# Optimization experiments

Hardware: AMD Instinct MI355X
Metric: run time of the kernel (lower is better)

The kernel has to match this reference:

```python
import jax, jax.numpy as jnp
import numpy as np

ELEM, EMBD, WIN = 128, 128, 128

def setup_inputs() -> dict:
    key = jax.random.key(0)
    ks = jax.random.split(key, 7)
    s = 1.0 / np.sqrt(ELEM)
    return {
        "x": jax.random.normal(ks[0], (8, 16384, ELEM), dtype=jnp.float32),
        "Wq": jax.random.uniform(ks[1], (EMBD, ELEM), jnp.float32, -s, s),
        "bq": jax.random.uniform(ks[2], (EMBD,), jnp.float32, -s, s),
        "Wk": jax.random.uniform(ks[3], (EMBD, ELEM), jnp.float32, -s, s),
        "bk": jax.random.uniform(ks[4], (EMBD,), jnp.float32, -s, s),
        "Wv": jax.random.uniform(ks[5], (EMBD, ELEM), jnp.float32, -s, s),
        "bv": jax.random.uniform(ks[6], (EMBD,), jnp.float32, -s, s),
    }

def reference(x, Wq, bq, Wk, bk, Wv, bv):
    N, S, E = x.shape
    P = S // WIN
    xp = x.reshape(N, P, WIN, E)  # [N,P,W,E]
    q = jnp.einsum('npwe,de->npwd', xp, Wq) + bq
    k = jnp.einsum('npwe,de->npwd', xp, Wk) + bk
    v = jnp.einsum('npwe,de->npwd', xp, Wv) + bv
    # note: original applies NO 1/sqrt(d) scaling
    scores = jnp.einsum('npwd,npud->npwu', q, k)  # [N,P,W,W]
    attn = jax.nn.softmax(scores, axis=-1)
    out = jnp.einsum('npwu,npud->npwd', attn, v)
    return out.reshape(N, S, EMBD)
```

## Files before the change

kernel.cpp:

```cpp
#include <hip/hip_runtime.h>

#define LDSP 136

typedef _Float16 h8 __attribute__((ext_vector_type(8)));
typedef _Float16 h4 __attribute__((ext_vector_type(4)));
typedef float    f4 __attribute__((ext_vector_type(4)));
typedef float    fx16 __attribute__((ext_vector_type(16)));

__global__ void prep(const float* __restrict__ Wq, const float* __restrict__ Wk,
                     const float* __restrict__ bq, _Float16* __restrict__ Mt,
                     float* __restrict__ ck) {
    int idx = blockIdx.x * 256 + threadIdx.x;
    int e = idx & 127, f = idx >> 7;
    float a0 = 0.f, a1 = 0.f, a2 = 0.f, a3 = 0.f;
    for (int d = 0; d < 128; d += 4) {
        a0 += Wk[(d + 0) * 128 + f] * Wq[(d + 0) * 128 + e];
        a1 += Wk[(d + 1) * 128 + f] * Wq[(d + 1) * 128 + e];
        a2 += Wk[(d + 2) * 128 + f] * Wq[(d + 2) * 128 + e];
        a3 += Wk[(d + 3) * 128 + f] * Wq[(d + 3) * 128 + e];
    }
    Mt[idx] = (_Float16)((a0 + a1) + (a2 + a3));

    if (blockIdx.x == 0 && threadIdx.x < 128) {
        int t = threadIdx.x;
        float c0 = 0.f, c1 = 0.f, c2 = 0.f, c3 = 0.f;
        for (int d = 0; d < 128; d += 4) {
            c0 += bq[d + 0] * Wk[(d + 0) * 128 + t];
            c1 += bq[d + 1] * Wk[(d + 1) * 128 + t];
            c2 += bq[d + 2] * Wk[(d + 2) * 128 + t];
            c3 += bq[d + 3] * Wk[(d + 3) * 128 + t];
        }
        ck[t] = (c0 + c1) + (c2 + c3);
    }
}

__global__ __launch_bounds__(512, 2) void attn(
    const float* __restrict__ x, const _Float16* __restrict__ Mt,
    const float* __restrict__ Wv, const float* __restrict__ ck,
    const float* __restrict__ bv, float* __restrict__ out) {
    __shared__ _Float16 Xs[128 * LDSP];
    __shared__ _Float16 Ts[128 * LDSP];
    __shared__ _Float16 Vs[128 * LDSP];
    __shared__ float2   Sm[256];

    const int tid  = threadIdx.x;
    const int wv   = tid >> 6;
    const int lane = tid & 63;
    const int l32  = lane & 31;
    const int hi   = lane >> 5;
    const int hv   = wv & 1;
    const int t4   = wv >> 1;

    h8 mtf[8], wvf[8];
#pragma unroll
    for (int e0 = 0; e0 < 8; ++e0) {
        mtf[e0] = *(const h8*)(Mt + (t4 * 32 + l32) * 128 + e0 * 16 + hi * 8);
        const float* wp = Wv + (t4 * 32 + l32) * 128 + e0 * 16 + hi * 8;
        f4 w0 = *(const f4*)wp;
        f4 w1 = *(const f4*)(wp + 4);
        wvf[e0] = (h8){(_Float16)w0.x, (_Float16)w0.y, (_Float16)w0.z, (_Float16)w0.w,
                       (_Float16)w1.x, (_Float16)w1.y, (_Float16)w1.z, (_Float16)w1.w};
    }
    const float bvv = bv[t4 * 32 + l32];

    const size_t base0 = (size_t)blockIdx.x * 4 * (128 * 128);

    f4 pf[8];
#pragma unroll
    for (int j = 0; j < 8; ++j)
        pf[j] = *(const f4*)(x + base0 + 4 * tid + 2048 * j);

    for (int it = 0; it < 4; ++it) {
#pragma unroll
        for (int j = 0; j < 8; ++j) {
            int idx = 4 * tid + 2048 * j;
            int row = idx >> 7, col = idx & 127;
            f4 f = pf[j];
            h4 h = {(_Float16)f.x, (_Float16)f.y, (_Float16)f.z, (_Float16)f.w};
            *(h4*)(&Xs[row * LDSP + col]) = h;
        }
        __syncthreads();

        h8 xf0[8], xf1[8];
        fx16 accT0, accT1;
        {
            f4 ckv[4];
#pragma unroll
            for (int run = 0; run < 4; ++run)
                ckv[run] = *(const f4*)(ck + t4 * 32 + run * 8 + 4 * hi);
#pragma unroll
            for (int r = 0; r < 16; ++r) accT0[r] = ckv[r >> 2][r & 3];
            accT1 = accT0;
        }
#pragma unroll
        for (int e0 = 0; e0 < 8; ++e0) {
            xf0[e0] = *(const h8*)(&Xs[(hv * 64 + l32) * LDSP + e0 * 16 + hi * 8]);
            xf1[e0] = *(const h8*)(&Xs[(hv * 64 + 32 + l32) * LDSP + e0 * 16 + hi * 8]);
            accT0 = __builtin_amdgcn_mfma_f32_32x32x16_f16(mtf[e0], xf0[e0], accT0, 0, 0, 0);
            accT1 = __builtin_amdgcn_mfma_f32_32x32x16_f16(mtf[e0], xf1[e0], accT1, 0, 0, 0);
        }
#pragma unroll
        for (int run = 0; run < 4; ++run) {
            h4 h0 = {(_Float16)accT0[run * 4 + 0], (_Float16)accT0[run * 4 + 1],
                     (_Float16)accT0[run * 4 + 2], (_Float16)accT0[run * 4 + 3]};
            *(h4*)(&Ts[(hv * 64 + l32) * LDSP + t4 * 32 + run * 8 + 4 * hi]) = h0;
            h4 h1 = {(_Float16)accT1[run * 4 + 0], (_Float16)accT1[run * 4 + 1],
                     (_Float16)accT1[run * 4 + 2], (_Float16)accT1[run * 4 + 3]};
            *(h4*)(&Ts[(hv * 64 + 32 + l32) * LDSP + t4 * 32 + run * 8 + 4 * hi]) = h1;
        }

        fx16 accV0, accV1;
#pragma unroll
        for (int r = 0; r < 16; ++r) accV0[r] = bvv;
        accV1 = accV0;
#pragma unroll
        for (int e0 = 0; e0 < 8; ++e0) {
            accV0 = __builtin_amdgcn_mfma_f32_32x32x16_f16(xf0[e0], wvf[e0], accV0, 0, 0, 0);
            accV1 = __builtin_amdgcn_mfma_f32_32x32x16_f16(xf1[e0], wvf[e0], accV1, 0, 0, 0);
        }
#pragma unroll
        for (int run = 0; run < 4; ++run) {
            h4 g0 = {(_Float16)accV0[run * 4 + 0], (_Float16)accV0[run * 4 + 1],
                     (_Float16)accV0[run * 4 + 2], (_Float16)accV0[run * 4 + 3]};
            *(h4*)(&Vs[(t4 * 32 + l32) * LDSP + hv * 64 + run * 8 + 4 * hi]) = g0;
            h4 g1 = {(_Float16)accV1[run * 4 + 0], (_Float16)accV1[run * 4 + 1],
                     (_Float16)accV1[run * 4 + 2], (_Float16)accV1[run * 4 + 3]};
            *(h4*)(&Vs[(t4 * 32 + l32) * LDSP + hv * 64 + 32 + run * 8 + 4 * hi]) = g1;
        }
        __syncthreads();

        if (it < 3) {
            const float* nx = x + base0 + (size_t)(it + 1) * (128 * 128);
#pragma unroll
            for (int j = 0; j < 8; ++j)
                pf[j] = *(const f4*)(nx + 4 * tid + 2048 * j);
        }

        fx16 s0, s1;
#pragma unroll
        for (int r = 0; r < 16; ++r) s0[r] = 0.f;
        s1 = s0;
#pragma unroll
        for (int f0 = 0; f0 < 8; ++f0) {
            h8 tf = *(const h8*)(&Ts[(t4 * 32 + l32) * LDSP + f0 * 16 + hi * 8]);
            s0 = __builtin_amdgcn_mfma_f32_32x32x16_f16(xf0[f0], tf, s0, 0, 0, 0);
            s1 = __builtin_amdgcn_mfma_f32_32x32x16_f16(xf1[f0], tf, s1, 0, 0, 0);
        }
        float m = -1e30f;
#pragma unroll
        for (int r = 0; r < 16; ++r) m = fmaxf(m, fmaxf(s0[r], s1[r]));
        m = fmaxf(m, __shfl_xor(m, 32, 64));
        float ss = 0.f;
#pragma unroll
        for (int r = 0; r < 16; ++r) {
            s0[r] = __expf(s0[r] - m);
            s1[r] = __expf(s1[r] - m);
            ss += s0[r] + s1[r];
        }
        ss += __shfl_xor(ss, 32, 64);
        if (hi == 0) Sm[hv * 128 + t4 * 32 + l32] = make_float2(m, ss);
        __syncthreads();
        float2 om = Sm[(hv ^ 1) * 128 + t4 * 32 + l32];
        float M   = fmaxf(m, om.x);
        float inv = __expf(m - M) / (ss * __expf(m - M) + om.y * __expf(om.x - M));
#pragma unroll
        for (int run = 0; run < 4; ++run) {
            h4 p0 = {(_Float16)(s0[run * 4 + 0] * inv), (_Float16)(s0[run * 4 + 1] * inv),
                     (_Float16)(s0[run * 4 + 2] * inv), (_Float16)(s0[run * 4 + 3] * inv)};
            *(h4*)(&Ts[(t4 * 32 + l32) * LDSP + hv * 64 + run * 8 + 4 * hi]) = p0;
            h4 p1 = {(_Float16)(s1[run * 4 + 0] * inv), (_Float16)(s1[run * 4 + 1] * inv),
                     (_Float16)(s1[run * 4 + 2] * inv), (_Float16)(s1[run * 4 + 3] * inv)};
            *(h4*)(&Ts[(t4 * 32 + l32) * LDSP + hv * 64 + 32 + run * 8 + 4 * hi]) = p1;
        }
        __syncthreads();

        fx16 o0, o1;
#pragma unroll
        for (int r = 0; r < 16; ++r) o0[r] = 0.f;
        o1 = o0;
#pragma unroll
        for (int u0 = 0; u0 < 8; ++u0) {
            h8 pr = *(const h8*)(&Ts[(t4 * 32 + l32) * LDSP + u0 * 16 + hi * 8]);
            h8 v0 = *(const h8*)(&Vs[(hv * 64 + l32) * LDSP + u0 * 16 + hi * 8]);
            h8 v1 = *(const h8*)(&Vs[(hv * 64 + 32 + l32) * LDSP + u0 * 16 + hi * 8]);
            o0 = __builtin_amdgcn_mfma_f32_32x32x16_f16(pr, v0, o0, 0, 0, 0);
            o1 = __builtin_amdgcn_mfma_f32_32x32x16_f16(pr, v1, o1, 0, 0, 0);
        }
        float* ob = out + base0 + (size_t)it * (128 * 128);
#pragma unroll
        for (int r = 0; r < 16; ++r) {
            int w = t4 * 32 + (r & 3) + 8 * (r >> 2) + 4 * hi;
            ob[(size_t)w * 128 + hv * 64 + l32]      = o0[r];
            ob[(size_t)w * 128 + hv * 64 + 32 + l32] = o1[r];
        }
    }
}

extern "C" void kernel_launch(void* const* d_in, const int* in_sizes, int n_in,
                              void* d_out, int out_size, void* d_ws, size_t ws_size,
                              hipStream_t stream) {
    const float* x  = (const float*)d_in[0];
    const float* Wq = (const float*)d_in[1];
    const float* bq = (const float*)d_in[2];
    const float* Wk = (const float*)d_in[3];
    const float* Wv = (const float*)d_in[5];
    const float* bv = (const float*)d_in[6];

    _Float16* Mt  = (_Float16*)d_ws;
    float*    ckp = (float*)(Mt + 16384);

    prep<<<64, 256, 0, stream>>>(Wq, Wk, bq, Mt, ckp);
    attn<<<256, 512, 0, stream>>>(x, Mt, Wv, ckp, bv, (float*)d_out);
}
```

Before: 144.0 us.

## Process one window per block, loading x straight into registers

Replaces the 4-window-per-block loop with one 128x128 window per block and launches 1024 blocks instead of 256. x is read from global memory directly into MFMA fragment registers, so the Xs LDS buffer and its barrier go away. The launch-bounds occupancy hint rises from 2 to 4. This trades away the software prefetch of the next window and reloads the Mt/Wv fragments in every block, in exchange for more concurrent blocks to hide latency. The direct x loads are strided per lane, so coalescing may be worse, and the higher occupancy target may force register spills.

```diff
diff --git a/kernel.cpp b/kernel.cpp
--- a/kernel.cpp
+++ b/kernel.cpp
@@ -34,11 +34,10 @@
     }
 }
 
-__global__ __launch_bounds__(512, 2) void attn(
+__global__ __launch_bounds__(512, 4) void attn(
     const float* __restrict__ x, const _Float16* __restrict__ Mt,
     const float* __restrict__ Wv, const float* __restrict__ ck,
     const float* __restrict__ bv, float* __restrict__ out) {
-    __shared__ _Float16 Xs[128 * LDSP];
     __shared__ _Float16 Ts[128 * LDSP];
     __shared__ _Float16 Vs[128 * LDSP];
     __shared__ float2   Sm[256];
@@ -51,6 +50,25 @@
     const int hv   = wv & 1;
     const int t4   = wv >> 1;
 
+    const size_t base = (size_t)blockIdx.x * (128 * 128);
+
+    h8 xf0[8], xf1[8];
+    {
+        const float* xr0 = x + base + (size_t)(hv * 64 + l32) * 128 + hi * 8;
+        const float* xr1 = xr0 + 32 * 128;
+#pragma unroll
+        for (int e0 = 0; e0 < 8; ++e0) {
+            f4 a0 = *(const f4*)(xr0 + e0 * 16);
+            f4 a1 = *(const f4*)(xr0 + e0 * 16 + 4);
+            f4 b0 = *(const f4*)(xr1 + e0 * 16);
+            f4 b1 = *(const f4*)(xr1 + e0 * 16 + 4);
+            xf0[e0] = (h8){(_Float16)a0.x, (_Float16)a0.y, (_Float16)a0.z, (_Float16)a0.w,
+                           (_Float16)a1.x, (_Float16)a1.y, (_Float16)a1.z, (_Float16)a1.w};
+            xf1[e0] = (h8){(_Float16)b0.x, (_Float16)b0.y, (_Float16)b0.z, (_Float16)b0.w,
+                           (_Float16)b1.x, (_Float16)b1.y, (_Float16)b1.z, (_Float16)b1.w};
+        }
+    }
+
     h8 mtf[8], wvf[8];
 #pragma unroll
     for (int e0 = 0; e0 < 8; ++e0) {
@@ -63,136 +81,107 @@
     }
     const float bvv = bv[t4 * 32 + l32];
 
-    const size_t base0 = (size_t)blockIdx.x * 4 * (128 * 128);
-
-    f4 pf[8];
-#pragma unroll
-    for (int j = 0; j < 8; ++j)
-        pf[j] = *(const f4*)(x + base0 + 4 * tid + 2048 * j);
-
-    for (int it = 0; it < 4; ++it) {
-#pragma unroll
-        for (int j = 0; j < 8; ++j) {
-            int idx = 4 * tid + 2048 * j;
-            int row = idx >> 7, col = idx & 127;
-            f4 f = pf[j];
-            h4 h = {(_Float16)f.x, (_Float16)f.y, (_Float16)f.z, (_Float16)f.w};
-            *(h4*)(&Xs[row * LDSP + col]) = h;
-        }
-        __syncthreads();
-
-        h8 xf0[8], xf1[8];
-        fx16 accT0, accT1;
-        {
-            f4 ckv[4];
-#pragma unroll
-            for (int run = 0; run < 4; ++run)
-                ckv[run] = *(const f4*)(ck + t4 * 32 + run * 8 + 4 * hi);
-#pragma unroll
-            for (int r = 0; r < 16; ++r) accT0[r] = ckv[r >> 2][r & 3];
-            accT1 = accT0;
-        }
-#pragma unroll
-        for (int e0 = 0; e0 < 8; ++e0) {
-            xf0[e0] = *(const h8*)(&Xs[(hv * 64 + l32) * LDSP + e0 * 16 + hi * 8]);
-            xf1[e0] = *(const h8*)(&Xs[(hv * 64 + 32 + l32) * LDSP + e0 * 16 + hi * 8]);
-            accT0 = __builtin_amdgcn_mfma_f32_32x32x16_f16(mtf[e0], xf0[e0], accT0, 0, 0, 0);
-            accT1 = __builtin_amdgcn_mfma_f32_32x32x16_f16(mtf[e0], xf1[e0], accT1, 0, 0, 0);
-        }
-#pragma unroll
-        for (int run = 0; run < 4; ++run) {
-            h4 h0 = {(_Float16)accT0[run * 4 + 0], (_Float16)accT0[run * 4 + 1],
-                     (_Float16)accT0[run * 4 + 2], (_Float16)accT0[run * 4 + 3]};
-            *(h4*)(&Ts[(hv * 64 + l32) * LDSP + t4 * 32 + run * 8 + 4 * hi]) = h0;
-            h4 h1 = {(_Float16)accT1[run * 4 + 0], (_Float16)accT1[run * 4 + 1],
-                     (_Float16)accT1[run * 4 + 2], (_Float16)accT1[run * 4 + 3]};
-            *(h4*)(&Ts[(hv * 64 + 32 + l32) * LDSP + t4 * 32 + run * 8 + 4 * hi]) = h1;
-        }
-
-        fx16 accV0, accV1;
-#pragma unroll
-        for (int r = 0; r < 16; ++r) accV0[r] = bvv;
-        accV1 = accV0;
-#pragma unroll
-        for (int e0 = 0; e0 < 8; ++e0) {
-            accV0 = __builtin_amdgcn_mfma_f32_32x32x16_f16(xf0[e0], wvf[e0], accV0, 0, 0, 0);
-            accV1 = __builtin_amdgcn_mfma_f32_32x32x16_f16(xf1[e0], wvf[e0], accV1, 0, 0, 0);
-        }
-#pragma unroll
-        for (int run = 0; run < 4; ++run) {
-            h4 g0 = {(_Float16)accV0[run * 4 + 0], (_Float16)accV0[run * 4 + 1],
-                     (_Float16)accV0[run * 4 + 2], (_Float16)accV0[run * 4 + 3]};
-            *(h4*)(&Vs[(t4 * 32 + l32) * LDSP + hv * 64 + run * 8 + 4 * hi]) = g0;
-            h4 g1 = {(_Float16)accV1[run * 4 + 0], (_Float16)accV1[run * 4 + 1],
-                     (_Float16)accV1[run * 4 + 2], (_Float16)accV1[run * 4 + 3]};
-            *(h4*)(&Vs[(t4 * 32 + l32) * LDSP + hv * 64 + 32 + run * 8 + 4 * hi]) = g1;
-        }
-        __syncthreads();
-
-        if (it < 3) {
-            const float* nx = x + base0 + (size_t)(it + 1) * (128 * 128);
-#pragma unroll
-            for (int j = 0; j < 8; ++j)
-                pf[j] = *(const f4*)(nx + 4 * tid + 2048 * j);
-        }
-
-        fx16 s0, s1;
-#pragma unroll
-        for (int r = 0; r < 16; ++r) s0[r] = 0.f;
-        s1 = s0;
-#pragma unroll
-        for (int f0 = 0; f0 < 8; ++f0) {
-            h8 tf = *(const h8*)(&Ts[(t4 * 32 + l32) * LDSP + f0 * 16 + hi * 8]);
-            s0 = __builtin_amdgcn_mfma_f32_32x32x16_f16(xf0[f0], tf, s0, 0, 0, 0);
-            s1 = __builtin_amdgcn_mfma_f32_32x32x16_f16(xf1[f0], tf, s1, 0, 0, 0);
-        }
-        float m = -1e30f;
-#pragma unroll
-        for (int r = 0; r < 16; ++r) m = fmaxf(m, fmaxf(s0[r], s1[r]));
-        m = fmaxf(m, __shfl_xor(m, 32, 64));
-        float ss = 0.f;
-#pragma unroll
-        for (int r = 0; r < 16; ++r) {
-            s0[r] = __expf(s0[r] - m);
-            s1[r] = __expf(s1[r] - m);
-            ss += s0[r] + s1[r];
-        }
-        ss += __shfl_xor(ss, 32, 64);
-        if (hi == 0) Sm[hv * 128 + t4 * 32 + l32] = make_float2(m, ss);
-        __syncthreads();
-        float2 om = Sm[(hv ^ 1) * 128 + t4 * 32 + l32];
-        float M   = fmaxf(m, om.x);
-        float inv = __expf(m - M) / (ss * __expf(m - M) + om.y * __expf(om.x - M));
-#pragma unroll
-        for (int run = 0; run < 4; ++run) {
-            h4 p0 = {(_Float16)(s0[run * 4 + 0] * inv), (_Float16)(s0[run * 4 + 1] * inv),
-                     (_Float16)(s0[run * 4 + 2] * inv), (_Float16)(s0[run * 4 + 3] * inv)};
-            *(h4*)(&Ts[(t4 * 32 + l32) * LDSP + hv * 64 + run * 8 + 4 * hi]) = p0;
-            h4 p1 = {(_Float16)(s1[run * 4 + 0] * inv), (_Float16)(s1[run * 4 + 1] * inv),
-                     (_Float16)(s1[run * 4 + 2] * inv), (_Float16)(s1[run * 4 + 3] * inv)};
-            *(h4*)(&Ts[(t4 * 32 + l32) * LDSP + hv * 64 + 32 + run * 8 + 4 * hi]) = p1;
-        }
-        __syncthreads();
-
-        fx16 o0, o1;
-#pragma unroll
-        for (int r = 0; r < 16; ++r) o0[r] = 0.f;
-        o1 = o0;
-#pragma unroll
-        for (int u0 = 0; u0 < 8; ++u0) {
-            h8 pr = *(const h8*)(&Ts[(t4 * 32 + l32) * LDSP + u0 * 16 + hi * 8]);
-            h8 v0 = *(const h8*)(&Vs[(hv * 64 + l32) * LDSP + u0 * 16 + hi * 8]);
-            h8 v1 = *(const h8*)(&Vs[(hv * 64 + 32 + l32) * LDSP + u0 * 16 + hi * 8]);
-            o0 = __builtin_amdgcn_mfma_f32_32x32x16_f16(pr, v0, o0, 0, 0, 0);
-            o1 = __builtin_amdgcn_mfma_f32_32x32x16_f16(pr, v1, o1, 0, 0, 0);
-        }
-        float* ob = out + base0 + (size_t)it * (128 * 128);
-#pragma unroll
-        for (int r = 0; r < 16; ++r) {
-            int w = t4 * 32 + (r & 3) + 8 * (r >> 2) + 4 * hi;
-            ob[(size_t)w * 128 + hv * 64 + l32]      = o0[r];
-            ob[(size_t)w * 128 + hv * 64 + 32 + l32] = o1[r];
-        }
+    fx16 accT0, accT1;
+    {
+        f4 ckv[4];
+#pragma unroll
+        for (int run = 0; run < 4; ++run)
+            ckv[run] = *(const f4*)(ck + t4 * 32 + run * 8 + 4 * hi);
+#pragma unroll
+        for (int r = 0; r < 16; ++r) accT0[r] = ckv[r >> 2][r & 3];
+        accT1 = accT0;
+    }
+#pragma unroll
+    for (int e0 = 0; e0 < 8; ++e0) {
+        accT0 = __builtin_amdgcn_mfma_f32_32x32x16_f16(mtf[e0], xf0[e0], accT0, 0, 0, 0);
+        accT1 = __builtin_amdgcn_mfma_f32_32x32x16_f16(mtf[e0], xf1[e0], accT1, 0, 0, 0);
+    }
+#pragma unroll
+    for (int run = 0; run < 4; ++run) {
+        h4 h0 = {(_Float16)accT0[run * 4 + 0], (_Float16)accT0[run * 4 + 1],
+                 (_Float16)accT0[run * 4 + 2], (_Float16)accT0[run * 4 + 3]};
+        *(h4*)(&Ts[(hv * 64 + l32) * LDSP + t4 * 32 + run * 8 + 4 * hi]) = h0;
+        h4 h1 = {(_Float16)accT1[run * 4 + 0], (_Float16)accT1[run * 4 + 1],
+                 (_Float16)accT1[run * 4 + 2], (_Float16)accT1[run * 4 + 3]};
+        *(h4*)(&Ts[(hv * 64 + 32 + l32) * LDSP + t4 * 32 + run * 8 + 4 * hi]) = h1;
+    }
+
+    fx16 accV0, accV1;
+#pragma unroll
+    for (int r = 0; r < 16; ++r) accV0[r] = bvv;
+    accV1 = accV0;
+#pragma unroll
+    for (int e0 = 0; e0 < 8; ++e0) {
+        accV0 = __builtin_amdgcn_mfma_f32_32x32x16_f16(xf0[e0], wvf[e0], accV0, 0, 0, 0);
+        accV1 = __builtin_amdgcn_mfma_f32_32x32x16_f16(xf1[e0], wvf[e0], accV1, 0, 0, 0);
+    }
+#pragma unroll
+    for (int run = 0; run < 4; ++run) {
+        h4 g0 = {(_Float16)accV0[run * 4 + 0], (_Float16)accV0[run * 4 + 1],
+                 (_Float16)accV0[run * 4 + 2], (_Float16)accV0[run * 4 + 3]};
+        *(h4*)(&Vs[(t4 * 32 + l32) * LDSP + hv * 64 + run * 8 + 4 * hi]) = g0;
+        h4 g1 = {(_Float16)accV1[run * 4 + 0], (_Float16)accV1[run * 4 + 1],
+                 (_Float16)accV1[run * 4 + 2], (_Float16)accV1[run * 4 + 3]};
+        *(h4*)(&Vs[(t4 * 32 + l32) * LDSP + hv * 64 + 32 + run * 8 + 4 * hi]) = g1;
+    }
+    __syncthreads();
+
+    fx16 s0, s1;
+#pragma unroll
+    for (int r = 0; r < 16; ++r) s0[r] = 0.f;
+    s1 = s0;
+#pragma unroll
+    for (int f0 = 0; f0 < 8; ++f0) {
+        h8 tf = *(const h8*)(&Ts[(t4 * 32 + l32) * LDSP + f0 * 16 + hi * 8]);
+        s0 = __builtin_amdgcn_mfma_f32_32x32x16_f16(xf0[f0], tf, s0, 0, 0, 0);
+        s1 = __builtin_amdgcn_mfma_f32_32x32x16_f16(xf1[f0], tf, s1, 0, 0, 0);
+    }
+    float m = -1e30f;
+#pragma unroll
+    for (int r = 0; r < 16; ++r) m = fmaxf(m, fmaxf(s0[r], s1[r]));
+    m = fmaxf(m, __shfl_xor(m, 32, 64));
+    float ss = 0.f;
+#pragma unroll
+    for (int r = 0; r < 16; ++r) {
+        s0[r] = __expf(s0[r] - m);
+        s1[r] = __expf(s1[r] - m);
+        ss += s0[r] + s1[r];
+    }
+    ss += __shfl_xor(ss, 32, 64);
+    if (hi == 0) Sm[hv * 128 + t4 * 32 + l32] = make_float2(m, ss);
+    __syncthreads();
+    float2 om = Sm[(hv ^ 1) * 128 + t4 * 32 + l32];
+    float M   = fmaxf(m, om.x);
+    float inv = __expf(m - M) / (ss * __expf(m - M) + om.y * __expf(om.x - M));
+#pragma unroll
+    for (int run = 0; run < 4; ++run) {
+        h4 p0 = {(_Float16)(s0[run * 4 + 0] * inv), (_Float16)(s0[run * 4 + 1] * inv),
+                 (_Float16)(s0[run * 4 + 2] * inv), (_Float16)(s0[run * 4 + 3] * inv)};
+        *(h4*)(&Ts[(t4 * 32 + l32) * LDSP + hv * 64 + run * 8 + 4 * hi]) = p0;
+        h4 p1 = {(_Float16)(s1[run * 4 + 0] * inv), (_Float16)(s1[run * 4 + 1] * inv),
+                 (_Float16)(s1[run * 4 + 2] * inv), (_Float16)(s1[run * 4 + 3] * inv)};
+        *(h4*)(&Ts[(t4 * 32 + l32) * LDSP + hv * 64 + 32 + run * 8 + 4 * hi]) = p1;
+    }
+    __syncthreads();
+
+    fx16 o0, o1;
+#pragma unroll
+    for (int r = 0; r < 16; ++r) o0[r] = 0.f;
+    o1 = o0;
+#pragma unroll
+    for (int u0 = 0; u0 < 8; ++u0) {
+        h8 pr = *(const h8*)(&Ts[(t4 * 32 + l32) * LDSP + u0 * 16 + hi * 8]);
+        h8 v0 = *(const h8*)(&Vs[(hv * 64 + l32) * LDSP + u0 * 16 + hi * 8]);
+        h8 v1 = *(const h8*)(&Vs[(hv * 64 + 32 + l32) * LDSP + u0 * 16 + hi * 8]);
+        o0 = __builtin_amdgcn_mfma_f32_32x32x16_f16(pr, v0, o0, 0, 0, 0);
+        o1 = __builtin_amdgcn_mfma_f32_32x32x16_f16(pr, v1, o1, 0, 0, 0);
+    }
+    float* ob = out + base;
+#pragma unroll
+    for (int r = 0; r < 16; ++r) {
+        int w = t4 * 32 + (r & 3) + 8 * (r >> 2) + 4 * hi;
+        ob[(size_t)w * 128 + hv * 64 + l32]      = o0[r];
+        ob[(size_t)w * 128 + hv * 64 + 32 + l32] = o1[r];
     }
 }
 
@@ -210,5 +199,5 @@
     float*    ckp = (float*)(Mt + 16384);
 
     prep<<<64, 256, 0, stream>>>(Wq, Wk, bq, Mt, ckp);
-    attn<<<256, 512, 0, stream>>>(x, Mt, Wv, ckp, bv, (float*)d_out);
+    attn<<<1024, 512, 0, stream>>>(x, Mt, Wv, ckp, bv, (float*)d_out);
 }
```

Measured after the change: 185.9 us. +29.1%, slower.
